# Performance work log

Hardware: AMD Instinct MI355X
Metric: run time of the kernel (lower is better)

Reference implementation:

```python
import jax, jax.numpy as jnp
import numpy as np

DECAY = 0.99
EPS = 1e-05


def setup_inputs() -> dict:
    key = jax.random.key(0)
    k1, k2, k3 = jax.random.split(key, 3)
    return {
        "input": jax.random.normal(k1, (32, 64, 64, 64), dtype=jnp.float32),
        "embed": jax.random.normal(k2, (64, 512), dtype=jnp.float32),
        "cluster_size": jnp.zeros((512,), dtype=jnp.float32),
        "embed_avg": jax.random.normal(k3, (64, 512), dtype=jnp.float32),
    }


def reference(input, embed, cluster_size, embed_avg):
    n_embed = embed.shape[1]
    flatten = input.reshape(-1, input.shape[-1])  # [N, dim]
    dist = (
        jnp.sum(flatten * flatten, axis=1, keepdims=True)
        - 2.0 * flatten @ embed
        + jnp.sum(embed * embed, axis=0, keepdims=True)
    )  # [N, n_embed]
    embed_ind_flat = jnp.argmin(dist, axis=1)  # [N]
    embed_ind = embed_ind_flat.reshape(input.shape[:-1])
    quantize = jnp.take(embed.T, embed_ind_flat, axis=0).reshape(input.shape)
    diff = jnp.mean((quantize - input) ** 2)

    # EMA codebook update (training path; buffer updates returned as outputs)
    embed_onehot_sum = jnp.zeros((n_embed,), dtype=flatten.dtype).at[embed_ind_flat].add(1.0)
    embed_sum = jax.ops.segment_sum(flatten, embed_ind_flat, num_segments=n_embed).T  # [dim, n_embed]
    new_cluster_size = cluster_size * DECAY + (1.0 - DECAY) * embed_onehot_sum
    new_embed_avg = embed_avg * DECAY + (1.0 - DECAY) * embed_sum
    n = jnp.sum(new_cluster_size)
    cs = (new_cluster_size + EPS) / (n + n_embed * EPS) * n
    new_embed = new_embed_avg / cs[None, :]

    # straight-through estimator
    quantize_st = input + jax.lax.stop_gradient(quantize - input)
    return (quantize_st, diff, embed_ind, new_embed, new_cluster_size, new_embed_avg)
```

## Files before the change

kernel.cpp:

```cpp
#include <hip/hip_runtime.h>

#define DIM     64
#define N_EMBED 512
#define N_ROWS  131072
#define XPAD    132

__global__ void prep_kernel(const float* __restrict__ embed,
                            float* __restrict__ se,
                            float* __restrict__ embed_t,
                            int do_et) {
    int j = blockIdx.x * blockDim.x + threadIdx.x;
    if (j >= N_EMBED) return;
    float s = 0.f;
#pragma unroll
    for (int d = 0; d < DIM; d += 4) {
        float b0 = embed[(d + 0) * N_EMBED + j];
        float b1 = embed[(d + 1) * N_EMBED + j];
        float b2 = embed[(d + 2) * N_EMBED + j];
        float b3 = embed[(d + 3) * N_EMBED + j];
        s = fmaf(b0, b0, s); s = fmaf(b1, b1, s);
        s = fmaf(b2, b2, s); s = fmaf(b3, b3, s);
        if (do_et) {
            float4 v; v.x = b0; v.y = b1; v.z = b2; v.w = b3;
            *reinterpret_cast<float4*>(&embed_t[j * DIM + d]) = v;
        }
    }
    se[j] = s;
}

__launch_bounds__(256, 2)
__global__ void vq_assign(const float* __restrict__ input,
                          const float* __restrict__ embed,
                          const float* __restrict__ se,
                          const float* __restrict__ embed_t,
                          float* __restrict__ out_ind,
                          int*   __restrict__ ind,
                          float* __restrict__ out_q,
                          double* __restrict__ diff_acc,
                          int have_et) {
    __shared__ float Xs[64][XPAD];
    __shared__ float Es[64][XPAD];
    __shared__ float sxs[128];
    __shared__ int   bjs[128];
    __shared__ float wsum2[4];

    const int t    = threadIdx.x;
    const int row0 = blockIdx.x * 128;
    const int tr   = t >> 4;
    const int tc   = t & 15;
    const int bx   = ((tc >> 2) & 1) * 4;

#pragma unroll
    for (int ph = 0; ph < 8; ++ph) {
        int idx = ph * 256 + t;
        int row = idx >> 4;
        int kq  = idx & 15;
        float4 v = *reinterpret_cast<const float4*>(
            &input[(size_t)(row0 + row) * 64 + kq * 4]);
        Xs[kq * 4 + 0][row] = v.x;
        Xs[kq * 4 + 1][row] = v.y;
        Xs[kq * 4 + 2][row] = v.z;
        Xs[kq * 4 + 3][row] = v.w;
    }
    __syncthreads();

    if (t < 128) {
        float s = 0.f;
#pragma unroll 8
        for (int k = 0; k < 64; ++k) { float x = Xs[k][t]; s = fmaf(x, x, s); }
        sxs[t] = s;
    }

    float bestd[8], sx[8];
    int   bestj[8];
#pragma unroll
    for (int r = 0; r < 8; ++r) { bestd[r] = INFINITY; bestj[r] = 0; }

    for (int chunk = 0; chunk < 4; ++chunk) {
        const int ccb = chunk * 128;
        __syncthreads();
#pragma unroll
        for (int ph = 0; ph < 8; ++ph) {
            int idx = ph * 256 + t;
            int k   = idx >> 5;
            int cq  = idx & 31;
            float4 v = *reinterpret_cast<const float4*>(
                &embed[k * N_EMBED + ccb + cq * 4]);
            *reinterpret_cast<float4*>(&Es[k][(cq * 4) ^ (((cq >> 3) & 1) * 4)]) = v;
        }
        __syncthreads();
        if (chunk == 0) {
#pragma unroll
            for (int r = 0; r < 8; ++r) sx[r] = sxs[tr * 8 + r];
        }

        float acc[8][8];
#pragma unroll
        for (int r = 0; r < 8; ++r)
#pragma unroll
            for (int c = 0; c < 8; ++c) acc[r][c] = 0.f;

#pragma unroll 2
        for (int k = 0; k < 64; ++k) {
            float a[8], b[8];
            *reinterpret_cast<float4*>(&a[0]) = *reinterpret_cast<const float4*>(&Xs[k][tr * 8]);
            *reinterpret_cast<float4*>(&a[4]) = *reinterpret_cast<const float4*>(&Xs[k][tr * 8 + 4]);
            *reinterpret_cast<float4*>(&b[0]) = *reinterpret_cast<const float4*>(&Es[k][(tc * 8) ^ bx]);
            *reinterpret_cast<float4*>(&b[4]) = *reinterpret_cast<const float4*>(&Es[k][(tc * 8 + 4) ^ bx]);
#pragma unroll
            for (int r = 0; r < 8; ++r)
#pragma unroll
                for (int c = 0; c < 8; ++c)
                    acc[r][c] = fmaf(a[r], b[c], acc[r][c]);
        }

#pragma unroll
        for (int c = 0; c < 8; ++c) {
            int j = ccb + tc * 8 + c;
            float sej = se[j];
#pragma unroll
            for (int r = 0; r < 8; ++r) {
                float d = (sx[r] - 2.f * acc[r][c]) + sej;
                if (d < bestd[r]) { bestd[r] = d; bestj[r] = j; }
            }
        }
    }

    __syncthreads();
    float* rd = &Es[0][0];
    int*   rj = (int*)(rd + 128 * 17);
#pragma unroll
    for (int r = 0; r < 8; ++r) {
        rd[(tr * 8 + r) * 17 + tc] = bestd[r];
        rj[(tr * 8 + r) * 17 + tc] = bestj[r];
    }
    __syncthreads();
    if (t < 128) {
        float bd = rd[t * 17 + 0];
        int   bj = rj[t * 17 + 0];
#pragma unroll
        for (int w = 1; w < 16; ++w) {
            float dw = rd[t * 17 + w];
            int   jw = rj[t * 17 + w];
            if (dw < bd || (dw == bd && jw < bj)) { bd = dw; bj = jw; }
        }
        out_ind[row0 + t] = (float)bj;
        ind[row0 + t]     = bj;
        bjs[t]            = bj;
    }
    __syncthreads();

    const int erow  = t >> 1;
    const int ehalf = t & 1;
    const int grow  = row0 + erow;
    const int bj2   = bjs[erow];
    const float* xr = input + (size_t)grow * DIM + ehalf * 32;
    float*       oq = out_q + (size_t)grow * DIM + ehalf * 32;
    float dsum = 0.f;

    if (have_et) {
        const float* er = embed_t + (size_t)bj2 * DIM + ehalf * 32;
#pragma unroll
        for (int i = 0; i < 32; i += 4) {
            float4 xv = *reinterpret_cast<const float4*>(xr + i);
            float4 ev = *reinterpret_cast<const float4*>(er + i);
            float t0 = ev.x - xv.x, t1 = ev.y - xv.y;
            float t2 = ev.z - xv.z, t3 = ev.w - xv.w;
            float4 o;
            o.x = xv.x + t0; o.y = xv.y + t1; o.z = xv.z + t2; o.w = xv.w + t3;
            *reinterpret_cast<float4*>(oq + i) = o;
            dsum = fmaf(t0, t0, dsum); dsum = fmaf(t1, t1, dsum);
            dsum = fmaf(t2, t2, dsum); dsum = fmaf(t3, t3, dsum);
        }
    } else {
#pragma unroll
        for (int i = 0; i < 32; ++i) {
            float x = xr[i];
            float e = embed[(ehalf * 32 + i) * N_EMBED + bj2];
            float t0 = e - x;
            oq[i] = x + t0;
            dsum = fmaf(t0, t0, dsum);
        }
    }

    for (int off = 32; off > 0; off >>= 1) dsum += __shfl_down(dsum, off, 64);
    int lane = t & 63, wid = t >> 6;
    if (lane == 0) wsum2[wid] = dsum;
    __syncthreads();
    if (t == 0) {
        float b = wsum2[0] + wsum2[1] + wsum2[2] + wsum2[3];
        atomicAdd(diff_acc, (double)b);
    }
}

__launch_bounds__(256, 4)
__global__ void vq_esum(const float* __restrict__ input,
                        const int* __restrict__ ind,
                        float* __restrict__ esum,
                        int* __restrict__ gcount) {
    const int dimg = blockIdx.x & 7;
    const int rowg = blockIdx.x >> 3;
    const int t    = threadIdx.x;
    const int w    = t >> 6;
    const int lane = t & 63;
    const int rloc = lane >> 3;
    const int d    = lane & 7;

    __shared__ float tab[8][513];
    __shared__ int   lcnt[N_EMBED];

    for (int i = t; i < 8 * 513; i += 256) (&tab[0][0])[i] = 0.f;
    if (dimg == 0) { lcnt[t] = 0; lcnt[t + 256] = 0; }
    __syncthreads();

    const int rbase = rowg * 2048;
    const int dbase = dimg * 8;

#pragma unroll 4
    for (int it = 0; it < 64; ++it) {
        const int row = rbase + it * 32 + w * 8 + rloc;
        const int j = ind[row];
        const float x = input[(size_t)row * DIM + dbase + d];
        atomicAdd(&tab[d][j], x);
        if (dimg == 0 && d == 0) atomicAdd(&lcnt[j], 1);
    }
    __syncthreads();

    for (int i = t; i < 8 * N_EMBED; i += 256) {
        const int dl = i >> 9, j = i & 511;
        float v = tab[dl][j];
        if (v != 0.f) atomicAdd(&esum[(dbase + dl) * N_EMBED + j], v);
    }
    if (dimg == 0) {
        int v0 = lcnt[t];       if (v0) atomicAdd(&gcount[t], v0);
        int v1 = lcnt[t + 256]; if (v1) atomicAdd(&gcount[t + 256], v1);
    }
}

__global__ void fin_a(const float* __restrict__ cluster_size,
                      const int* __restrict__ gcount,
                      float* __restrict__ out_ncs,
                      float* __restrict__ nstore) {
    int t = threadIdx.x;
    float ncs = cluster_size[t] * 0.99f + 0.01f * (float)gcount[t];
    out_ncs[t] = ncs;
    __shared__ float red[512];
    red[t] = ncs;
    __syncthreads();
    for (int s = 256; s > 0; s >>= 1) {
        if (t < s) red[t] += red[t + s];
        __syncthreads();
    }
    if (t == 0) nstore[0] = red[0];
}

__global__ void fin_b(const float* __restrict__ embed_avg,
                      const float* __restrict__ esum,
                      const float* __restrict__ out_ncs,
                      const float* __restrict__ nstore,
                      const double* __restrict__ diff_acc,
                      float* __restrict__ out_ne,
                      float* __restrict__ out_nea,
                      float* __restrict__ out_diff) {
    int e = blockIdx.x * 512 + threadIdx.x;
    const float EPSF = 1e-5f;
    float n = nstore[0];
    int j = e & (N_EMBED - 1);
    float ncs = out_ncs[j];
    float cs = (ncs + EPSF) / (n + 512.0f * EPSF) * n;
    float es = embed_avg[e] * 0.99f + 0.01f * esum[e];
    out_nea[e] = es;
    out_ne[e] = es / cs;
    if (e == 0) out_diff[0] = (float)(*diff_acc * (1.0 / 8388608.0));
}

extern "C" void kernel_launch(void* const* d_in, const int* in_sizes, int n_in,
                              void* d_out, int out_size, void* d_ws, size_t ws_size,
                              hipStream_t stream) {
    const float* input        = (const float*)d_in[0];
    const float* embed        = (const float*)d_in[1];
    const float* cluster_size = (const float*)d_in[2];
    const float* embed_avg    = (const float*)d_in[3];

    float* out_q    = (float*)d_out;
    float* out_diff = out_q + 8388608;
    float* out_ind  = out_diff + 1;
    float* out_ne   = out_ind + 131072;
    float* out_ncs  = out_ne + 32768;
    float* out_nea  = out_ncs + 512;

    char*   ws       = (char*)d_ws;
    double* diff_acc = (double*)ws;
    float*  nstore   = (float*)(ws + 64);
    int*    gcount   = (int*)(ws + 256);
    float*  se       = (float*)(ws + 4096);
    int*    ind      = (int*)(ws + 8192);
    float*  esum     = (float*)(ws + 8192 + 524288);
    float*  embed_t  = (float*)(ws + 8192 + 524288 + 131072);

    const size_t need_et = 8192 + 524288 + 131072 + 131072;
    const int have_et = (ws_size >= need_et) ? 1 : 0;

    hipMemsetAsync(ws, 0, 4096, stream);
    hipMemsetAsync(ws + 8192 + 524288, 0, 131072, stream);

    prep_kernel<<<2, 256, 0, stream>>>(embed, se, embed_t, have_et);
    vq_assign<<<1024, 256, 0, stream>>>(input, embed, se, embed_t, out_ind, ind,
                                        out_q, diff_acc, have_et);
    vq_esum<<<512, 256, 0, stream>>>(input, ind, esum, gcount);
    fin_a<<<1, 512, 0, stream>>>(cluster_size, gcount, out_ncs, nstore);
    fin_b<<<64, 512, 0, stream>>>(embed_avg, esum, out_ncs, nstore, diff_acc,
                                  out_ne, out_nea, out_diff);
}
```

Before: 262.5 us.

## Replace shared-memory segment-sum tables with direct global atomics in transposed layout

The codebook sum kernel no longer builds per-block 8x512 shared-memory tables over 2048 rows. It now launches 2048 blocks of 64 rows each, and every row's 64 dims are atomically added straight into a code-major esum buffer ([code][dim]) so that each wave's atomics are contiguous. The finalize kernel reads esum with the transposed index. This removes the table zeroing, the flush pass and the low-parallelism launch, but it sends 8M global float atomics to L2, where contention on popular codes could serialize.

```diff
diff --git a/kernel.cpp b/kernel.cpp
--- a/kernel.cpp
+++ b/kernel.cpp
@@ -193,47 +193,35 @@
     }
 }
 
-__launch_bounds__(256, 4)
-__global__ void vq_esum(const float* __restrict__ input,
-                        const int* __restrict__ ind,
-                        float* __restrict__ esum,
-                        int* __restrict__ gcount) {
-    const int dimg = blockIdx.x & 7;
-    const int rowg = blockIdx.x >> 3;
+__launch_bounds__(256)
+__global__ void vq_esum3(const float* __restrict__ input,
+                         const int* __restrict__ ind,
+                         float* __restrict__ esum,
+                         int* __restrict__ gcount) {
+    __shared__ int js[64];
+    __shared__ int lcnt[N_EMBED];
     const int t    = threadIdx.x;
     const int w    = t >> 6;
     const int lane = t & 63;
-    const int rloc = lane >> 3;
-    const int d    = lane & 7;
-
-    __shared__ float tab[8][513];
-    __shared__ int   lcnt[N_EMBED];
-
-    for (int i = t; i < 8 * 513; i += 256) (&tab[0][0])[i] = 0.f;
-    if (dimg == 0) { lcnt[t] = 0; lcnt[t + 256] = 0; }
-    __syncthreads();
-
-    const int rbase = rowg * 2048;
-    const int dbase = dimg * 8;
-
-#pragma unroll 4
-    for (int it = 0; it < 64; ++it) {
-        const int row = rbase + it * 32 + w * 8 + rloc;
-        const int j = ind[row];
-        const float x = input[(size_t)row * DIM + dbase + d];
-        atomicAdd(&tab[d][j], x);
-        if (dimg == 0 && d == 0) atomicAdd(&lcnt[j], 1);
-    }
-    __syncthreads();
-
-    for (int i = t; i < 8 * N_EMBED; i += 256) {
-        const int dl = i >> 9, j = i & 511;
-        float v = tab[dl][j];
-        if (v != 0.f) atomicAdd(&esum[(dbase + dl) * N_EMBED + j], v);
-    }
-    if (dimg == 0) {
-        int v0 = lcnt[t];       if (v0) atomicAdd(&gcount[t], v0);
-        int v1 = lcnt[t + 256]; if (v1) atomicAdd(&gcount[t + 256], v1);
+    const int rbase = blockIdx.x * 64;
+
+    lcnt[t] = 0; lcnt[t + 256] = 0;
+    if (t < 64) js[t] = ind[rbase + t];
+    __syncthreads();
+    if (t < 64) atomicAdd(&lcnt[js[t]], 1);
+
+#pragma unroll
+    for (int r = 0; r < 16; ++r) {
+        const int rl = w * 16 + r;
+        const int j = js[rl];
+        const float x = input[(size_t)(rbase + rl) * DIM + lane];
+        atomicAdd(&esum[j * DIM + lane], x);
+    }
+    __syncthreads();
+
+    for (int i = t; i < N_EMBED; i += 256) {
+        int v = lcnt[i];
+        if (v) atomicAdd(&gcount[i], v);
     }
 }
 
@@ -265,10 +253,11 @@
     int e = blockIdx.x * 512 + threadIdx.x;
     const float EPSF = 1e-5f;
     float n = nstore[0];
+    int d = e >> 9;
     int j = e & (N_EMBED - 1);
     float ncs = out_ncs[j];
     float cs = (ncs + EPSF) / (n + 512.0f * EPSF) * n;
-    float es = embed_avg[e] * 0.99f + 0.01f * esum[e];
+    float es = embed_avg[e] * 0.99f + 0.01f * esum[j * DIM + d];
     out_nea[e] = es;
     out_ne[e] = es / cs;
     if (e == 0) out_diff[0] = (float)(*diff_acc * (1.0 / 8388608.0));
@@ -307,7 +296,7 @@
     prep_kernel<<<2, 256, 0, stream>>>(embed, se, embed_t, have_et);
     vq_assign<<<1024, 256, 0, stream>>>(input, embed, se, embed_t, out_ind, ind,
                                         out_q, diff_acc, have_et);
-    vq_esum<<<512, 256, 0, stream>>>(input, ind, esum, gcount);
+    vq_esum3<<<2048, 256, 0, stream>>>(input, ind, esum, gcount);
     fin_a<<<1, 512, 0, stream>>>(cluster_size, gcount, out_ncs, nstore);
     fin_b<<<64, 512, 0, stream>>>(embed_avg, esum, out_ncs, nstore, diff_acc,
                                   out_ne, out_nea, out_diff);
```

Result: slower. 383.8 us (+46.2%).
